# Kernel tuning notes

Measured on AMD Instinct MI355X. Metric: run time of the kernel, lower is better.

Reference implementation:

```python
import jax, jax.numpy as jnp
import numpy as np

A, B, NB = 100_000, 200_000, 6      # atoms, directed bonds, max neighbors
FA, FB, H = 133, 147, 256            # atom fdim, bond fdim, hidden
M, DEPTH = 5_000, 4                  # molecules, message-passing depth


def setup_inputs() -> dict:
    key = jax.random.key(0)
    ks = jax.random.split(key, 12)
    f_atoms = jax.random.normal(ks[0], (A, FA), jnp.float32)
    f_bonds = jax.random.normal(ks[1], (B, FB), jnp.float32)
    a2b = jax.random.randint(ks[2], (A, NB), 0, B, dtype=jnp.int32)
    b2a = jax.random.randint(ks[3], (B,), 0, A, dtype=jnp.int32)
    b2revb = jax.random.randint(ks[4], (B,), 0, B, dtype=jnp.int32)
    # weights (bias=False per args.bias, except W_o which always has bias)
    W_ia = jax.random.normal(ks[5], (FA, H), jnp.float32) / np.sqrt(FA)
    W_ib = jax.random.normal(ks[6], (FB, H), jnp.float32) / np.sqrt(FB)
    W_h = jax.random.normal(ks[7], (DEPTH - 1, H, H), jnp.float32) / np.sqrt(H)
    W_o = jax.random.normal(ks[8], (H, H), jnp.float32) / np.sqrt(H)
    b_o = jax.random.normal(ks[9], (H,), jnp.float32) * 0.01
    W_lr = jax.random.normal(ks[10], (3 * H, H), jnp.float32) / np.sqrt(3 * H)
    # ragged molecule sizes summing exactly to A (avg 20 atoms/mol)
    rng = np.random.default_rng(0)
    sizes = (A // M) + rng.integers(-5, 6, M)
    sizes[-1] += A - sizes.sum()
    sizes = jnp.asarray(sizes, jnp.int32)
    return dict(f_atoms=f_atoms, f_bonds=f_bonds, W_ia=W_ia, W_ib=W_ib,
                W_h=W_h, W_o=W_o, b_o=b_o, W_lr=W_lr,
                a2b=a2b, b2a=b2a, b2revb=b2revb, sizes=sizes)


def _sum_max_agg(message_bond, a2b):
    nei = message_bond[a2b]                 # [A, NB, H] gather
    return nei.sum(axis=1) * nei.max(axis=1)


def reference(f_atoms, f_bonds, W_ia, W_ib, W_h, W_o, b_o, W_lr,
              a2b, b2a, b2revb, sizes):
    input_atom = jax.nn.relu(f_atoms @ W_ia)    # [A, H]
    message_atom = input_atom
    input_bond = jax.nn.relu(f_bonds @ W_ib)    # [B, H]
    message_bond = input_bond
    for d in range(DEPTH - 1):
        agg = _sum_max_agg(message_bond, a2b)          # [A, H]
        message_atom = message_atom + agg
        rev = message_bond[b2revb]                     # [B, H]
        message_bond = message_atom[b2a] - rev
        message_bond = jax.nn.relu(input_bond + message_bond @ W_h[d])
        # dropout p=0.0 -> identity
    agg = _sum_max_agg(message_bond, a2b)              # [A, H]
    agg = jnp.concatenate([agg, message_atom, input_atom], axis=1) @ W_lr
    atom_hiddens = jax.nn.relu(agg @ W_o + b_o)        # [A, H]
    # ragged per-molecule mean pooling (a_scope)
    mol_ids = jnp.repeat(jnp.arange(M), sizes, total_repeat_length=A)
    sums = jax.ops.segment_sum(atom_hiddens, mol_ids, num_segments=M)
    mol_vecs = sums / sizes[:, None].astype(atom_hiddens.dtype)
    return mol_vecs                                    # [M, H]
```

## Files before the change

kernel.cpp:

```cpp
#include <hip/hip_runtime.h>


typedef _Float16 f16;
typedef f16 f16x4 __attribute__((ext_vector_type(4)));
typedef __attribute__((ext_vector_type(8))) short bh8;
typedef __attribute__((ext_vector_type(4))) float f32x4;

#define MB_SCALE 0.000244140625f
#define MB_INV   4096.0f
#define AGG_INV  16777216.0f

__device__ __forceinline__ unsigned short f2bf_rne(float f) {
    unsigned u = __float_as_uint(f);
    unsigned r = (u + 0x7fffu + ((u >> 16) & 1u)) >> 16;
    return (unsigned short)r;
}
__device__ __forceinline__ float bfu2f(unsigned short u) {
    return __uint_as_float(((unsigned)u) << 16);
}
__device__ __forceinline__ f32x4 mfma16(bh8 a, bh8 b, f32x4 c) {
    return __builtin_amdgcn_mfma_f32_16x16x32_bf16(a, b, c, 0, 0, 0);
}

__global__ __launch_bounds__(256) void wprep_kernel(
    const float* __restrict__ Wia, const float* __restrict__ Wib,
    const float* __restrict__ Wh,  const float* __restrict__ Wlr,
    const float* __restrict__ Wo,  short* __restrict__ ws)
{
    short* WiaT_hi = ws;
    short* WiaT_lo = ws + 40960;
    short* WibT_hi = ws + 81920;
    short* WibT_lo = ws + 122880;
    short* WhT_hi  = ws + 163840;
    short* WhT_lo  = ws + 360448;
    short* WlrT_hi = ws + 557056;
    short* WlrT_lo = ws + 753664;
    short* WoT_hi  = ws + 950272;
    short* WoT_lo  = ws + 1015808;

    int idx = blockIdx.x * 256 + threadIdx.x;
    float v; short *ph, *pl; int o;
    if (idx < 40960) {
        int n = idx / 160, k = idx - n * 160;
        v = (k < 133) ? Wia[(size_t)k * 256 + n] : 0.f;
        ph = WiaT_hi; pl = WiaT_lo; o = idx;
    } else if (idx < 81920) {
        int j = idx - 40960;
        int n = j / 160, k = j - n * 160;
        v = (k < 147) ? Wib[(size_t)k * 256 + n] : 0.f;
        ph = WibT_hi; pl = WibT_lo; o = j;
    } else if (idx < 278528) {
        int j = idx - 81920;
        int d = j >> 16, rem = j & 65535, n = rem >> 8, k = rem & 255;
        v = Wh[(size_t)d * 65536 + (size_t)k * 256 + n];
        ph = WhT_hi; pl = WhT_lo; o = j;
    } else if (idx < 475136) {
        int j = idx - 278528;
        int n = j / 768, k = j - n * 768;
        v = Wlr[(size_t)k * 256 + n];
        ph = WlrT_hi; pl = WlrT_lo; o = j;
    } else if (idx < 540672) {
        int j = idx - 475136;
        int n = j >> 8, k = j & 255;
        v = Wo[(size_t)k * 256 + n];
        ph = WoT_hi; pl = WoT_lo; o = j;
    } else return;
    unsigned short hb = f2bf_rne(v);
    ph[o] = (short)hb;
    pl[o] = (short)f2bf_rne(v - bfu2f(hb));
}

template <int KPAD, int SRC, int EPI>
__global__ __launch_bounds__(512, 4) void mfma_gemm(
    const void* __restrict__ a0, const void* __restrict__ a1,
    const void* __restrict__ a2,
    const short* __restrict__ Bhi, const short* __restrict__ Blo,
    const float* __restrict__ bias, void* __restrict__ outv,
    int M, int Kact)
{
    __shared__ short As_hi[128 * 40];
    __shared__ short As_lo[(SRC == 2) ? 8 : 128 * 40];

    const int tid  = threadIdx.x;
    const int lane = tid & 63;
    const int w    = tid >> 6;
    const int wm   = (w >> 2) * 64;
    const int wn   = (w & 3) * 64;
    const int row0 = blockIdx.x * 128;

    const int sm = tid >> 2;
    const int sk = (tid & 3) * 8;
    const int fm = lane & 15;
    const int fk = (lane >> 4) * 8;

    int grow = row0 + sm; if (grow > M - 1) grow = M - 1;

    f32x4 acc[4][4];
#pragma unroll
    for (int i = 0; i < 4; ++i)
#pragma unroll
        for (int j = 0; j < 4; ++j) {
            f32x4 z = {0.f, 0.f, 0.f, 0.f};
            acc[i][j] = z;
        }

    for (int k0 = 0; k0 < KPAD; k0 += 32) {
        __syncthreads();
        int base = sm * 40 + sk;
        if (SRC == 0) {
            const float* xrow = (const float*)a0 + (size_t)grow * Kact;
            bh8 h0, l0;
#pragma unroll
            for (int j = 0; j < 8; ++j) {
                int kc = k0 + sk + j;
                float v = (kc < Kact) ? xrow[kc] : 0.f;
                unsigned short hb = f2bf_rne(v);
                h0[j] = (short)hb; l0[j] = (short)f2bf_rne(v - bfu2f(hb));
            }
            *(bh8*)&As_hi[base] = h0;
            *(bh8*)&As_lo[base] = l0;
        } else if (SRC == 1) {
            if (k0 < 512) {
                const float* src = (k0 < 256) ? (const float*)a0 : (const float*)a1;
                int kl = k0 & 255;
                const float4* p = (const float4*)(src + (size_t)grow * 256 + kl + sk);
                float va[8];
#pragma unroll
                for (int q = 0; q < 2; ++q) {
                    float4 f = p[q];
                    va[q * 4 + 0] = f.x; va[q * 4 + 1] = f.y;
                    va[q * 4 + 2] = f.z; va[q * 4 + 3] = f.w;
                }
                bh8 h0, l0;
#pragma unroll
                for (int j = 0; j < 8; ++j) {
                    unsigned short hb = f2bf_rne(va[j]);
                    h0[j] = (short)hb; l0[j] = (short)f2bf_rne(va[j] - bfu2f(hb));
                }
                *(bh8*)&As_hi[base] = h0;
                *(bh8*)&As_lo[base] = l0;
            } else {
                const short* ia = (const short*)a2 + (size_t)grow * 256 + (k0 - 512) + sk;
                bh8 z;
#pragma unroll
                for (int j = 0; j < 8; ++j) z[j] = 0;
                *(bh8*)&As_hi[base] = *(const bh8*)ia;
                *(bh8*)&As_lo[base] = z;
            }
        } else {
            const short* xr = (const short*)a0 + (size_t)grow * 256 + k0 + sk;
            *(bh8*)&As_hi[base] = *(const bh8*)xr;
        }
        __syncthreads();

        bh8 bhf[4], blf[4];
#pragma unroll
        for (int nt = 0; nt < 4; ++nt) {
            int n = wn + nt * 16 + fm;
            size_t off = (size_t)n * KPAD + k0 + fk;
            bhf[nt] = *(const bh8*)(Bhi + off);
            blf[nt] = *(const bh8*)(Blo + off);
        }
#pragma unroll
        for (int mt = 0; mt < 4; ++mt) {
            int abase = (wm + mt * 16 + fm) * 40 + fk;
            bh8 ah = *(const bh8*)&As_hi[abase];
#pragma unroll
            for (int nt = 0; nt < 4; ++nt) {
                acc[mt][nt] = mfma16(ah, bhf[nt], acc[mt][nt]);
                acc[mt][nt] = mfma16(ah, blf[nt], acc[mt][nt]);
            }
            if (SRC != 2) {
                bh8 al = *(const bh8*)&As_lo[abase];
#pragma unroll
                for (int nt = 0; nt < 4; ++nt)
                    acc[mt][nt] = mfma16(al, bhf[nt], acc[mt][nt]);
            }
        }
    }

#pragma unroll
    for (int mt = 0; mt < 4; ++mt) {
        int rbase = row0 + wm + mt * 16 + (lane >> 4) * 4;
#pragma unroll
        for (int nt = 0; nt < 4; ++nt) {
            int col = wn + nt * 16 + fm;
            float bc = (EPI == 4) ? bias[col] : 0.f;
#pragma unroll
            for (int r = 0; r < 4; ++r) {
                int row = rbase + r;
                if (row < M) {
                    size_t o = (size_t)row * 256 + col;
                    float v = acc[mt][nt][r];
                    if (EPI == 0)      ((float*)outv)[o] = fmaxf(v, 0.f);
                    else if (EPI == 1) ((unsigned short*)outv)[o] = f2bf_rne(fmaxf(v, 0.f));
                    else if (EPI == 2) ((f16*)outv)[o] = (f16)(fmaxf(v, 0.f) * MB_SCALE);
                    else if (EPI == 3) ((unsigned short*)outv)[o] = f2bf_rne(v);
                    else               ((float*)outv)[o] = fmaxf(v + bc, 0.f);
                }
            }
        }
    }
}

__global__ __launch_bounds__(512, 4) void bond_mfma_kernel(
    const float* __restrict__ FB,
    const short* __restrict__ WibT_hi, const short* __restrict__ WibT_lo,
    const short* __restrict__ WhT_hi,  const short* __restrict__ WhT_lo,
    const float* __restrict__ matom, const f16* __restrict__ mb_old,
    const int* __restrict__ b2a, const int* __restrict__ b2revb,
    f16* __restrict__ mb_new, int M)
{
    __shared__ short As[2][2][128 * 40];

    const int tid  = threadIdx.x;
    const int lane = tid & 63;
    const int w    = tid >> 6;
    const int wm   = (w >> 2) * 64;
    const int wn   = (w & 3) * 64;
    const int row0 = blockIdx.x * 128;

    const int sm = tid >> 2;
    const int sk = (tid & 3) * 8;

    int grow = row0 + sm; if (grow > M - 1) grow = M - 1;
    const float* frow = FB + (size_t)grow * 147;
    const float* arow = matom + (size_t)b2a[grow] * 256;
    const f16*   rrow = mb_old + (size_t)b2revb[grow] * 256;

    const int fm = lane & 15;
    const int fk = (lane >> 4) * 8;

    f32x4 acc[4][4];
#pragma unroll
    for (int i = 0; i < 4; ++i)
#pragma unroll
        for (int j = 0; j < 4; ++j) {
            f32x4 z = {0.f, 0.f, 0.f, 0.f};
            acc[i][j] = z;
        }

    float va[8];

    auto load = [&](int s) {
        if (s < 5) {
            int kb = s * 32 + sk;
#pragma unroll
            for (int j = 0; j < 8; ++j) {
                int kc = kb + j;
                va[j] = (kc < 147) ? frow[kc] : 0.f;
            }
        } else {
            int kb = (s - 5) * 32 + sk;
            const float4* ap = (const float4*)(arow + kb);
            const f16x4*  rp = (const f16x4*)(rrow + kb);
#pragma unroll
            for (int q = 0; q < 2; ++q) {
                float4 a = ap[q]; f16x4 r = rp[q];
                va[q * 4 + 0] = fmaf(-MB_INV, (float)r[0], a.x);
                va[q * 4 + 1] = fmaf(-MB_INV, (float)r[1], a.y);
                va[q * 4 + 2] = fmaf(-MB_INV, (float)r[2], a.z);
                va[q * 4 + 3] = fmaf(-MB_INV, (float)r[3], a.w);
            }
        }
    };
    auto store = [&](int buf) {
        bh8 h, l;
#pragma unroll
        for (int j = 0; j < 8; ++j) {
            unsigned short hb = f2bf_rne(va[j]);
            h[j] = (short)hb;
            l[j] = (short)f2bf_rne(va[j] - bfu2f(hb));
        }
        int base = sm * 40 + sk;
        *(bh8*)&As[buf][0][base] = h;
        *(bh8*)&As[buf][1][base] = l;
    };
    auto compute = [&](int buf, int s) {
        const short *Bh, *Bl; int ldb, k0;
        if (s < 5) { Bh = WibT_hi; Bl = WibT_lo; ldb = 160; k0 = s * 32; }
        else       { Bh = WhT_hi;  Bl = WhT_lo;  ldb = 256; k0 = (s - 5) * 32; }
        bh8 bhf[4], blf[4];
#pragma unroll
        for (int nt = 0; nt < 4; ++nt) {
            int n = wn + nt * 16 + fm;
            size_t off = (size_t)n * ldb + k0 + fk;
            bhf[nt] = *(const bh8*)(Bh + off);
            blf[nt] = *(const bh8*)(Bl + off);
        }
#pragma unroll
        for (int mt = 0; mt < 4; ++mt) {
            int abase = (wm + mt * 16 + fm) * 40 + fk;
            bh8 ah = *(const bh8*)&As[buf][0][abase];
            bh8 al = *(const bh8*)&As[buf][1][abase];
#pragma unroll
            for (int nt = 0; nt < 4; ++nt) {
                acc[mt][nt] = mfma16(ah, bhf[nt], acc[mt][nt]);
                acc[mt][nt] = mfma16(ah, blf[nt], acc[mt][nt]);
                acc[mt][nt] = mfma16(al, bhf[nt], acc[mt][nt]);
            }
        }
    };

    load(0);
    store(0);
    __syncthreads();

    int cur = 0;
    for (int s = 0; s < 13; ++s) {
        if (s < 12) load(s + 1);
        compute(cur, s);
        if (s == 4) {
#pragma unroll
            for (int i = 0; i < 4; ++i)
#pragma unroll
                for (int j = 0; j < 4; ++j)
#pragma unroll
                    for (int r = 0; r < 4; ++r)
                        acc[i][j][r] = fmaxf(acc[i][j][r], 0.f);
        }
        if (s < 12) store(cur ^ 1);
        __syncthreads();
        cur ^= 1;
    }

#pragma unroll
    for (int mt = 0; mt < 4; ++mt) {
        int rbase = row0 + wm + mt * 16 + (lane >> 4) * 4;
#pragma unroll
        for (int nt = 0; nt < 4; ++nt) {
            int col = wn + nt * 16 + fm;
#pragma unroll
            for (int r = 0; r < 4; ++r) {
                int row = rbase + r;
                if (row < M)
                    mb_new[(size_t)row * 256 + col] =
                        (f16)(fmaxf(acc[mt][nt][r], 0.f) * MB_SCALE);
            }
        }
    }
}

__global__ __launch_bounds__(256) void agg_kernel(
    const f16* __restrict__ mb, const int* __restrict__ a2b,
    float* __restrict__ matom, float* __restrict__ agg_out, int A)
{
    const int a    = blockIdx.x * 4 + (threadIdx.x >> 6);
    const int lane = threadIdx.x & 63;
    if (a >= A) return;
    const int* nb = a2b + (size_t)a * 6;

    f16x4 v0 = *(const f16x4*)(mb + (size_t)nb[0] * 256 + lane * 4);
    float s0 = (float)v0[0], s1 = (float)v0[1], s2 = (float)v0[2], s3 = (float)v0[3];
    float m0 = s0, m1 = s1, m2 = s2, m3 = s3;
#pragma unroll
    for (int j = 1; j < 6; ++j) {
        f16x4 v = *(const f16x4*)(mb + (size_t)nb[j] * 256 + lane * 4);
        float f0 = (float)v[0], f1 = (float)v[1], f2 = (float)v[2], f3 = (float)v[3];
        s0 += f0; s1 += f1; s2 += f2; s3 += f3;
        m0 = fmaxf(m0, f0); m1 = fmaxf(m1, f1);
        m2 = fmaxf(m2, f2); m3 = fmaxf(m3, f3);
    }
    size_t o = (size_t)a * 256 + lane * 4;
    if (agg_out) {
        float4 g = { AGG_INV * s0 * m0, AGG_INV * s1 * m1,
                     AGG_INV * s2 * m2, AGG_INV * s3 * m3 };
        *(float4*)(agg_out + o) = g;
    } else {
        float4 m = *(const float4*)(matom + o);
        m.x += AGG_INV * s0 * m0; m.y += AGG_INV * s1 * m1;
        m.z += AGG_INV * s2 * m2; m.w += AGG_INV * s3 * m3;
        *(float4*)(matom + o) = m;
    }
}

__global__ __launch_bounds__(256) void scan_kernel(
    const int* __restrict__ sizes, int* __restrict__ offsets, int M)
{
    __shared__ int part[256];
    const int t = threadIdx.x;
    const int chunk = (M + 255) / 256;
    int begin = t * chunk;
    int end = begin + chunk; if (end > M) end = M;
    int s = 0;
    for (int i = begin; i < end && i < M; ++i) s += sizes[i];
    part[t] = s;
    __syncthreads();
    for (int off = 1; off < 256; off <<= 1) {
        int v = (t >= off) ? part[t - off] : 0;
        __syncthreads();
        part[t] += v;
        __syncthreads();
    }
    int run = part[t] - s;
    for (int i = begin; i < end && i < M; ++i) { offsets[i] = run; run += sizes[i]; }
}

__global__ __launch_bounds__(256) void pool_kernel(
    const float* __restrict__ hid, const int* __restrict__ offsets,
    const int* __restrict__ sizes, float* __restrict__ out, int M, int A)
{
    const int m = blockIdx.x;
    const int h = threadIdx.x;
    int e = offsets[m];
    int sz = sizes[m];
    int start = e < A ? e : A;          if (start < 0) start = 0;
    int stop  = e + sz; if (stop > A) stop = A; if (stop < 0) stop = 0;
    float s = 0.f;
    for (int i = start; i < stop; ++i)
        s += hid[(size_t)i * 256 + h];
    out[(size_t)m * 256 + h] = s / (float)sz;
}

extern "C" void kernel_launch(void* const* d_in, const int* in_sizes, int n_in,
                              void* d_out, int out_size, void* d_ws, size_t ws_size,
                              hipStream_t stream)
{
    const float* f_atoms = (const float*)d_in[0];
    const float* f_bonds = (const float*)d_in[1];
    const float* W_ia    = (const float*)d_in[2];
    const float* W_ib    = (const float*)d_in[3];
    const float* W_h     = (const float*)d_in[4];
    const float* W_o     = (const float*)d_in[5];
    const float* b_o     = (const float*)d_in[6];
    const float* W_lr    = (const float*)d_in[7];
    const int*   a2b     = (const int*)d_in[8];
    const int*   b2a     = (const int*)d_in[9];
    const int*   b2revb  = (const int*)d_in[10];
    const int*   sizes   = (const int*)d_in[11];
    float* out = (float*)d_out;

    const int An = 100000, Bn = 200000, Mm = 5000;
    const size_t ABYTES = (size_t)An * 256 * 4;
    const size_t BBYTES = (size_t)Bn * 256 * 2;

    int*   offsets = (int*)d_ws;
    float* matom   = (float*)((char*)d_ws + 32768);
    f16*   mb0     = (f16*)((char*)matom + ABYTES);
    f16*   mb1     = (f16*)((char*)mb0 + BBYTES);
    short* wsplit  = (short*)((char*)mb1 + BBYTES);

    short* WiaT_hi = wsplit;
    short* WiaT_lo = wsplit + 40960;
    short* WibT_hi = wsplit + 81920;
    short* WibT_lo = wsplit + 122880;
    short* WhT_hi  = wsplit + 163840;
    short* WhT_lo  = wsplit + 360448;
    short* WlrT_hi = wsplit + 557056;
    short* WlrT_lo = wsplit + 753664;
    short* WoT_hi  = wsplit + 950272;
    short* WoT_lo  = wsplit + 1015808;

    dim3 blk(256);
    dim3 blk512(512);
    dim3 gA((An + 127) / 128, 1);
    dim3 gB((Bn + 127) / 128, 1);

    wprep_kernel<<<2112, blk, 0, stream>>>(W_ia, W_ib, W_h, W_lr, W_o, wsplit);

    mfma_gemm<160, 0, 0><<<gA, blk512, 0, stream>>>(
        f_atoms, nullptr, nullptr, WiaT_hi, WiaT_lo, nullptr, matom, An, 133);
    mfma_gemm<160, 0, 2><<<gB, blk512, 0, stream>>>(
        f_bonds, nullptr, nullptr, WibT_hi, WibT_lo, nullptr, mb0, Bn, 147);

    f16* cur = mb0; f16* nxt = mb1;
    for (int d = 0; d < 3; ++d) {
        agg_kernel<<<(An + 3) / 4, blk, 0, stream>>>(cur, a2b, matom, (float*)nullptr, An);
        bond_mfma_kernel<<<gB, blk512, 0, stream>>>(
            f_bonds, WibT_hi, WibT_lo,
            WhT_hi + (size_t)d * 65536, WhT_lo + (size_t)d * 65536,
            matom, cur, b2a, b2revb, nxt, Bn);
        f16* t = cur; cur = nxt; nxt = t;
    }

    float* aggbuf = (float*)mb0;
    agg_kernel<<<(An + 3) / 4, blk, 0, stream>>>(cur, a2b, matom, aggbuf, An);

    unsigned short* iatom = (unsigned short*)mb1;
    unsigned short* t1    = (unsigned short*)((char*)mb1 + 51200000);
    mfma_gemm<160, 0, 1><<<gA, blk512, 0, stream>>>(
        f_atoms, nullptr, nullptr, WiaT_hi, WiaT_lo, nullptr, iatom, An, 133);

    mfma_gemm<768, 1, 3><<<gA, blk512, 0, stream>>>(
        aggbuf, matom, iatom, WlrT_hi, WlrT_lo, nullptr, t1, An, 768);

    float* hid = (float*)mb0;
    mfma_gemm<256, 2, 4><<<gA, blk512, 0, stream>>>(
        t1, nullptr, nullptr, WoT_hi, WoT_lo, b_o, hid, An, 256);

    scan_kernel<<<1, 256, 0, stream>>>(sizes, offsets, Mm);
    pool_kernel<<<Mm, blk, 0, stream>>>(hid, offsets, sizes, out, Mm, An);
}
```

Before: 1.923 ms.

## Reuse stored input_bond and load bond-kernel fragments straight from global memory

The bond update kernel drops its shared-memory double buffer. Each wave now gathers its A fragments (matom[b2a] minus the reverse message) directly into registers, and the grid splits the 256 output columns across two blocks via blockIdx.y. For the first two depths the f_bonds @ W_ib GEMM is skipped: the stored fp16 input_bond buffer is read in the epilogue instead. Only the last depth, whose buffer was overwritten in place, recomputes that GEMM. This removes redundant K-steps and LDS barriers, but each block now gathers its rows twice, once per column half, and the reused input_bond carries fp16 precision.

```diff
diff --git a/kernel.cpp b/kernel.cpp
--- a/kernel.cpp
+++ b/kernel.cpp
@@ -3,6 +3,7 @@
 
 typedef _Float16 f16;
 typedef f16 f16x4 __attribute__((ext_vector_type(4)));
+typedef f16 f16x8 __attribute__((ext_vector_type(8)));
 typedef __attribute__((ext_vector_type(8))) short bh8;
 typedef __attribute__((ext_vector_type(4))) float f32x4;
 
@@ -203,33 +204,41 @@
     }
 }
 
-__global__ __launch_bounds__(512, 4) void bond_mfma_kernel(
+template <bool WITH_FB>
+__global__ __launch_bounds__(256, 2) void bond_frag_kernel(
     const float* __restrict__ FB,
     const short* __restrict__ WibT_hi, const short* __restrict__ WibT_lo,
     const short* __restrict__ WhT_hi,  const short* __restrict__ WhT_lo,
     const float* __restrict__ matom, const f16* __restrict__ mb_old,
+    const f16* __restrict__ ib,
     const int* __restrict__ b2a, const int* __restrict__ b2revb,
     f16* __restrict__ mb_new, int M)
 {
-    __shared__ short As[2][2][128 * 40];
-
     const int tid  = threadIdx.x;
     const int lane = tid & 63;
     const int w    = tid >> 6;
-    const int wm   = (w >> 2) * 64;
-    const int wn   = (w & 3) * 64;
+    const int wm   = (w >> 1) * 64;
+    const int wn   = (w & 1) * 64;
     const int row0 = blockIdx.x * 128;
-
-    const int sm = tid >> 2;
-    const int sk = (tid & 3) * 8;
-
-    int grow = row0 + sm; if (grow > M - 1) grow = M - 1;
-    const float* frow = FB + (size_t)grow * 147;
-    const float* arow = matom + (size_t)b2a[grow] * 256;
-    const f16*   rrow = mb_old + (size_t)b2revb[grow] * 256;
-
-    const int fm = lane & 15;
-    const int fk = (lane >> 4) * 8;
+    const int colb = blockIdx.y * 128;
+    const int fm   = lane & 15;
+    const int fk   = (lane >> 4) * 8;
+
+    const float *ap0, *ap1, *ap2, *ap3;
+    const f16 *rp0, *rp1, *rp2, *rp3;
+    const float *fp0, *fp1, *fp2, *fp3;
+    {
+        int r0 = row0 + wm + 0 * 16 + fm; if (r0 > M - 1) r0 = M - 1;
+        int r1 = row0 + wm + 1 * 16 + fm; if (r1 > M - 1) r1 = M - 1;
+        int r2 = row0 + wm + 2 * 16 + fm; if (r2 > M - 1) r2 = M - 1;
+        int r3 = row0 + wm + 3 * 16 + fm; if (r3 > M - 1) r3 = M - 1;
+        ap0 = matom + (size_t)b2a[r0] * 256; rp0 = mb_old + (size_t)b2revb[r0] * 256;
+        ap1 = matom + (size_t)b2a[r1] * 256; rp1 = mb_old + (size_t)b2revb[r1] * 256;
+        ap2 = matom + (size_t)b2a[r2] * 256; rp2 = mb_old + (size_t)b2revb[r2] * 256;
+        ap3 = matom + (size_t)b2a[r3] * 256; rp3 = mb_old + (size_t)b2revb[r3] * 256;
+        fp0 = FB + (size_t)r0 * 147; fp1 = FB + (size_t)r1 * 147;
+        fp2 = FB + (size_t)r2 * 147; fp3 = FB + (size_t)r3 * 147;
+    }
 
     f32x4 acc[4][4];
 #pragma unroll
@@ -240,88 +249,85 @@
             acc[i][j] = z;
         }
 
-    float va[8];
-
-    auto load = [&](int s) {
-        if (s < 5) {
-            int kb = s * 32 + sk;
+    if (WITH_FB) {
+        for (int s = 0; s < 5; ++s) {
+            int k0 = s * 32;
+            bh8 ah[4], al[4];
+#pragma unroll
+            for (int mt = 0; mt < 4; ++mt) {
+                const float* fp = (mt == 0) ? fp0 : (mt == 1) ? fp1 : (mt == 2) ? fp2 : fp3;
+#pragma unroll
+                for (int j = 0; j < 8; ++j) {
+                    int kc = k0 + fk + j;
+                    float v = (kc < 147) ? fp[kc] : 0.f;
+                    unsigned short hb = f2bf_rne(v);
+                    ah[mt][j] = (short)hb;
+                    al[mt][j] = (short)f2bf_rne(v - bfu2f(hb));
+                }
+            }
+#pragma unroll
+            for (int nt = 0; nt < 4; ++nt) {
+                int n = colb + wn + nt * 16 + fm;
+                size_t off = (size_t)n * 160 + k0 + fk;
+                bh8 bh = *(const bh8*)(WibT_hi + off);
+                bh8 bl = *(const bh8*)(WibT_lo + off);
+#pragma unroll
+                for (int mt = 0; mt < 4; ++mt) {
+                    acc[mt][nt] = mfma16(ah[mt], bh, acc[mt][nt]);
+                    acc[mt][nt] = mfma16(ah[mt], bl, acc[mt][nt]);
+                    acc[mt][nt] = mfma16(al[mt], bh, acc[mt][nt]);
+                }
+            }
+        }
+#pragma unroll
+        for (int i = 0; i < 4; ++i)
+#pragma unroll
+            for (int j = 0; j < 4; ++j)
+#pragma unroll
+                for (int r = 0; r < 4; ++r)
+                    acc[i][j][r] = fmaxf(acc[i][j][r], 0.f);
+    }
+
+#pragma unroll 2
+    for (int s = 0; s < 8; ++s) {
+        int k0 = s * 32;
+        bh8 ah[4], al[4];
+#pragma unroll
+        for (int mt = 0; mt < 4; ++mt) {
+            const float* ap = (mt == 0) ? ap0 : (mt == 1) ? ap1 : (mt == 2) ? ap2 : ap3;
+            const f16*   rp = (mt == 0) ? rp0 : (mt == 1) ? rp1 : (mt == 2) ? rp2 : rp3;
+            float4 a0 = *(const float4*)(ap + k0 + fk);
+            float4 a1 = *(const float4*)(ap + k0 + fk + 4);
+            f16x8  rv = *(const f16x8*)(rp + k0 + fk);
+            float va[8];
+            va[0] = fmaf(-MB_INV, (float)rv[0], a0.x);
+            va[1] = fmaf(-MB_INV, (float)rv[1], a0.y);
+            va[2] = fmaf(-MB_INV, (float)rv[2], a0.z);
+            va[3] = fmaf(-MB_INV, (float)rv[3], a0.w);
+            va[4] = fmaf(-MB_INV, (float)rv[4], a1.x);
+            va[5] = fmaf(-MB_INV, (float)rv[5], a1.y);
+            va[6] = fmaf(-MB_INV, (float)rv[6], a1.z);
+            va[7] = fmaf(-MB_INV, (float)rv[7], a1.w);
 #pragma unroll
             for (int j = 0; j < 8; ++j) {
-                int kc = kb + j;
-                va[j] = (kc < 147) ? frow[kc] : 0.f;
-            }
-        } else {
-            int kb = (s - 5) * 32 + sk;
-            const float4* ap = (const float4*)(arow + kb);
-            const f16x4*  rp = (const f16x4*)(rrow + kb);
-#pragma unroll
-            for (int q = 0; q < 2; ++q) {
-                float4 a = ap[q]; f16x4 r = rp[q];
-                va[q * 4 + 0] = fmaf(-MB_INV, (float)r[0], a.x);
-                va[q * 4 + 1] = fmaf(-MB_INV, (float)r[1], a.y);
-                va[q * 4 + 2] = fmaf(-MB_INV, (float)r[2], a.z);
-                va[q * 4 + 3] = fmaf(-MB_INV, (float)r[3], a.w);
-            }
-        }
-    };
-    auto store = [&](int buf) {
-        bh8 h, l;
-#pragma unroll
-        for (int j = 0; j < 8; ++j) {
-            unsigned short hb = f2bf_rne(va[j]);
-            h[j] = (short)hb;
-            l[j] = (short)f2bf_rne(va[j] - bfu2f(hb));
-        }
-        int base = sm * 40 + sk;
-        *(bh8*)&As[buf][0][base] = h;
-        *(bh8*)&As[buf][1][base] = l;
-    };
-    auto compute = [&](int buf, int s) {
-        const short *Bh, *Bl; int ldb, k0;
-        if (s < 5) { Bh = WibT_hi; Bl = WibT_lo; ldb = 160; k0 = s * 32; }
-        else       { Bh = WhT_hi;  Bl = WhT_lo;  ldb = 256; k0 = (s - 5) * 32; }
-        bh8 bhf[4], blf[4];
+                unsigned short hb = f2bf_rne(va[j]);
+                ah[mt][j] = (short)hb;
+                al[mt][j] = (short)f2bf_rne(va[j] - bfu2f(hb));
+            }
+        }
 #pragma unroll
         for (int nt = 0; nt < 4; ++nt) {
-            int n = wn + nt * 16 + fm;
-            size_t off = (size_t)n * ldb + k0 + fk;
-            bhf[nt] = *(const bh8*)(Bh + off);
-            blf[nt] = *(const bh8*)(Bl + off);
-        }
-#pragma unroll
-        for (int mt = 0; mt < 4; ++mt) {
-            int abase = (wm + mt * 16 + fm) * 40 + fk;
-            bh8 ah = *(const bh8*)&As[buf][0][abase];
-            bh8 al = *(const bh8*)&As[buf][1][abase];
-#pragma unroll
-            for (int nt = 0; nt < 4; ++nt) {
-                acc[mt][nt] = mfma16(ah, bhf[nt], acc[mt][nt]);
-                acc[mt][nt] = mfma16(ah, blf[nt], acc[mt][nt]);
-                acc[mt][nt] = mfma16(al, bhf[nt], acc[mt][nt]);
-            }
-        }
-    };
-
-    load(0);
-    store(0);
-    __syncthreads();
-
-    int cur = 0;
-    for (int s = 0; s < 13; ++s) {
-        if (s < 12) load(s + 1);
-        compute(cur, s);
-        if (s == 4) {
-#pragma unroll
-            for (int i = 0; i < 4; ++i)
-#pragma unroll
-                for (int j = 0; j < 4; ++j)
-#pragma unroll
-                    for (int r = 0; r < 4; ++r)
-                        acc[i][j][r] = fmaxf(acc[i][j][r], 0.f);
-        }
-        if (s < 12) store(cur ^ 1);
-        __syncthreads();
-        cur ^= 1;
+            int n = colb + wn + nt * 16 + fm;
+            size_t off = (size_t)n * 256 + k0 + fk;
+            bh8 bh = *(const bh8*)(WhT_hi + off);
+            bh8 bl = *(const bh8*)(WhT_lo + off);
+#pragma unroll
+            for (int mt = 0; mt < 4; ++mt) {
+                acc[mt][nt] = mfma16(ah[mt], bh, acc[mt][nt]);
+                acc[mt][nt] = mfma16(ah[mt], bl, acc[mt][nt]);
+                acc[mt][nt] = mfma16(al[mt], bh, acc[mt][nt]);
+            }
+        }
     }
 
 #pragma unroll
@@ -329,13 +335,16 @@
         int rbase = row0 + wm + mt * 16 + (lane >> 4) * 4;
 #pragma unroll
         for (int nt = 0; nt < 4; ++nt) {
-            int col = wn + nt * 16 + fm;
+            int col = colb + wn + nt * 16 + fm;
 #pragma unroll
             for (int r = 0; r < 4; ++r) {
                 int row = rbase + r;
-                if (row < M)
-                    mb_new[(size_t)row * 256 + col] =
-                        (f16)(fmaxf(acc[mt][nt][r], 0.f) * MB_SCALE);
+                if (row < M) {
+                    size_t o = (size_t)row * 256 + col;
+                    float v = acc[mt][nt][r];
+                    if (!WITH_FB) v = fmaf(MB_INV, (float)ib[o], v);
+                    mb_new[o] = (f16)(fmaxf(v, 0.f) * MB_SCALE);
+                }
             }
         }
     }
@@ -455,6 +464,7 @@
     dim3 blk512(512);
     dim3 gA((An + 127) / 128, 1);
     dim3 gB((Bn + 127) / 128, 1);
+    dim3 gF((Bn + 127) / 128, 2);
 
     wprep_kernel<<<2112, blk, 0, stream>>>(W_ia, W_ib, W_h, W_lr, W_o, wsplit);
 
@@ -463,18 +473,21 @@
     mfma_gemm<160, 0, 2><<<gB, blk512, 0, stream>>>(
         f_bonds, nullptr, nullptr, WibT_hi, WibT_lo, nullptr, mb0, Bn, 147);
 
-    f16* cur = mb0; f16* nxt = mb1;
-    for (int d = 0; d < 3; ++d) {
-        agg_kernel<<<(An + 3) / 4, blk, 0, stream>>>(cur, a2b, matom, (float*)nullptr, An);
-        bond_mfma_kernel<<<gB, blk512, 0, stream>>>(
-            f_bonds, WibT_hi, WibT_lo,
-            WhT_hi + (size_t)d * 65536, WhT_lo + (size_t)d * 65536,
-            matom, cur, b2a, b2revb, nxt, Bn);
-        f16* t = cur; cur = nxt; nxt = t;
-    }
+    agg_kernel<<<(An + 3) / 4, blk, 0, stream>>>(mb0, a2b, matom, (float*)nullptr, An);
+    bond_frag_kernel<false><<<gF, blk, 0, stream>>>(
+        f_bonds, WibT_hi, WibT_lo, WhT_hi, WhT_lo,
+        matom, mb0, mb0, b2a, b2revb, mb1, Bn);
+    agg_kernel<<<(An + 3) / 4, blk, 0, stream>>>(mb1, a2b, matom, (float*)nullptr, An);
+    bond_frag_kernel<false><<<gF, blk, 0, stream>>>(
+        f_bonds, WibT_hi, WibT_lo, WhT_hi + 65536, WhT_lo + 65536,
+        matom, mb1, mb0, b2a, b2revb, mb0, Bn);
+    agg_kernel<<<(An + 3) / 4, blk, 0, stream>>>(mb0, a2b, matom, (float*)nullptr, An);
+    bond_frag_kernel<true><<<gF, blk, 0, stream>>>(
+        f_bonds, WibT_hi, WibT_lo, WhT_hi + 131072, WhT_lo + 131072,
+        matom, mb0, nullptr, b2a, b2revb, mb1, Bn);
 
     float* aggbuf = (float*)mb0;
-    agg_kernel<<<(An + 3) / 4, blk, 0, stream>>>(cur, a2b, matom, aggbuf, An);
+    agg_kernel<<<(An + 3) / 4, blk, 0, stream>>>(mb1, a2b, matom, aggbuf, An);
 
     unsigned short* iatom = (unsigned short*)mb1;
     unsigned short* t1    = (unsigned short*)((char*)mb1 + 51200000);
```

Result: slower. 2.274 ms (+18.3%).
